# Performance work log

Measured on AMD Instinct MI355X. Metric: run time of the kernel, lower is better.

The kernel has to match this reference:

```python
import jax, jax.numpy as jnp
import numpy as np

EPS = 1e-8
LAM = 20.0  # lambda_softmax
I, R, T, W, D = 128, 48, 64, 100, 768


def l2norm(x, axis=-1):
    # matches torch l2norm: x / (sqrt(sum(x^2)) + eps)
    return x / (jnp.sqrt(jnp.sum(x * x, axis=axis, keepdims=True)) + EPS)


def _safe_div(num, den):
    return num / jnp.where(den > 0, den, 1.0)


def setup_inputs() -> dict:
    key = jax.random.key(0)
    k1, k2, k3, k4, k5 = jax.random.split(key, 5)
    return {
        "local_img_query": jax.random.normal(k1, (I, R, D), jnp.float32),
        "local_img_value": jax.random.normal(k2, (I, R, D), jnp.float32),
        "local_text_key": jax.random.normal(k3, (T, W, D), jnp.float32),
        "local_text_value": jax.random.normal(k4, (T, W, D), jnp.float32),
        "text_length": jax.random.randint(k5, (T,), 8, W + 1),
    }


def reference(local_img_query, local_img_value, local_text_key, local_text_value, text_length):
    # Vectorized over texts: padding words are masked instead of sliced,
    # reproducing the per-text ragged loop of compute_weiTexts exactly.
    Tn, Wn, Dn = local_text_key.shape
    In, Rn, _ = local_img_query.shape
    dtype = local_img_query.dtype
    mask = jnp.arange(Wn)[None, :] < text_length[:, None]          # [T,W] valid words
    Lf = text_length.astype(dtype)

    imgQn = l2norm(local_img_query)                                 # [I,R,D]
    txtKn = l2norm(local_text_key)                                  # [T,W,D]
    # cosine scores, shared by both directions (t2i uses the transpose)
    sim = jnp.einsum('twd,ird->tiwr', txtKn, imgQn)                 # [T,I,W,R]
    a = jax.nn.leaky_relu(sim, 0.1)

    # ---- i2t: query = image regions, source = text words ----
    ai = l2norm(a, axis=-1)                                         # l2norm over R per word row
    ai = jnp.swapaxes(ai, 2, 3)                                     # [T,I,R,W]
    m4 = mask[:, None, None, :]
    attn = jax.nn.softmax(jnp.where(m4, ai * LAM, -1e30), axis=-1)  # softmax over valid words
    attn = attn * m4
    # focal_equal with true source length L_i
    funcF = attn * Lf[:, None, None, None] - jnp.sum(attn, -1, keepdims=True)
    tmp = jnp.where(funcF > 0, attn, 0.0)
    attn = _safe_div(tmp, jnp.sum(tmp, -1, keepdims=True))
    weiText = l2norm(jnp.einsum('tirw,twd->tird', attn, local_text_value))  # [T,I,R,D]
    num = jnp.sum(local_img_value[None] * weiText, -1)
    den = jnp.maximum(jnp.linalg.norm(local_img_value, axis=-1)[None]
                      * jnp.linalg.norm(weiText, axis=-1), EPS)
    i2t = jnp.mean(num / den, axis=-1)                              # [T,I]

    # ---- t2i: query = text words, source = image regions ----
    a2 = jnp.swapaxes(a, 2, 3) * m4                                 # [T,I,R,W]; zero padded words before l2norm over W
    a2 = l2norm(a2, axis=-1)
    a2 = jnp.swapaxes(a2, 2, 3)                                     # [T,I,W,R]
    attn2 = jax.nn.softmax(a2 * LAM, axis=-1)                       # softmax over regions (dense)
    funcF2 = attn2 * Rn - jnp.sum(attn2, -1, keepdims=True)
    tmp2 = jnp.where(funcF2 > 0, attn2, 0.0)
    attn2 = _safe_div(tmp2, jnp.sum(tmp2, -1, keepdims=True))
    weiImage = l2norm(jnp.einsum('tiwr,ird->tiwd', attn2, local_img_value))  # [T,I,W,D]
    num2 = jnp.sum(local_text_value[:, None] * weiImage, -1)        # [T,I,W]
    den2 = jnp.maximum(jnp.linalg.norm(local_text_value, axis=-1)[:, None]
                       * jnp.linalg.norm(weiImage, axis=-1), EPS)
    sim2 = jnp.where(mask[:, None, :], num2 / den2, 0.0)
    t2i = jnp.sum(sim2, axis=-1) / Lf[:, None]                      # masked mean over valid words, [T,I]

    return i2t.T, t2i.T                                             # ([n_img,n_txt], [n_img,n_txt])
```

## Files before the change

### kernel.cpp

```cpp
#include <hip/hip_runtime.h>

#define EPS   1e-8f
#define LAMB  20.0f
#define NI    128
#define NR    48
#define NT    64
#define NW    100
#define ND    768

typedef unsigned int uint;
typedef unsigned short ushortt;
typedef __attribute__((ext_vector_type(8))) short short8;
typedef __attribute__((ext_vector_type(4))) float f32x4;

#define OFF_KHI  102400ULL
#define OFF_KLO  11112448ULL
#define OFF_QHI  22122496ULL
#define OFF_QLO  31559680ULL
#define OFF_TVB  40996864ULL
#define OFF_IVB  52006912ULL
#define OFF_MH   61444096ULL
#define OFF_ML   63279104ULL
#define OFF_HH   65114112ULL
#define OFF_HL   65900544ULL
#define WS_NEED  66686976ULL

__device__ inline unsigned short f2bf(float f) {
    uint u = __float_as_uint(f);
    u = (u + 0x7fffu + ((u >> 16) & 1u)) >> 16;
    return (unsigned short)u;
}
__device__ inline float bf2f(unsigned short h) {
    return __uint_as_float((uint)h << 16);
}
__device__ inline void split_store(float4 v, ushortt* hp, ushortt* lp) {
    unsigned short h0 = f2bf(v.x), h1 = f2bf(v.y), h2 = f2bf(v.z), h3 = f2bf(v.w);
    float f0 = bf2f(h0), f1 = bf2f(h1), f2 = bf2f(h2), f3 = bf2f(h3);
    ushort4 H; H.x = h0; H.y = h1; H.z = h2; H.w = h3;
    ushort4 L2; L2.x = f2bf(v.x - f0); L2.y = f2bf(v.y - f1); L2.z = f2bf(v.z - f2); L2.w = f2bf(v.w - f3);
    *(ushort4*)hp = H;
    *(ushort4*)lp = L2;
}
__device__ inline int swzATT(int r, int w) {
    return r * 128 + ((((w >> 3) ^ (r & 7)) << 3) | (w & 7));
}
__device__ inline int swzATT2(int w, int r) {
    return w * 64 + ((((r >> 3) ^ (w & 7)) << 3) | (r & 7));
}
__device__ inline float wredsum(float v) {
#pragma unroll
    for (int m = 1; m < 64; m <<= 1) v += __shfl_xor(v, m, 64);
    return v;
}
__device__ inline float wredmax(float v) {
#pragma unroll
    for (int m = 1; m < 64; m <<= 1) v = fmaxf(v, __shfl_xor(v, m, 64));
    return v;
}

__global__ void nafs_norms(const float* __restrict__ imgQ,
                           const float* __restrict__ imgV,
                           const float* __restrict__ txtK,
                           const float* __restrict__ txtV,
                           float* __restrict__ ws) {
    int row  = blockIdx.x * 4 + (threadIdx.x >> 6);
    int lane = threadIdx.x & 63;
    const float* src;
    int inv;
    if (row < 6144)       { src = imgQ + (size_t)row * ND;           inv = 1; }
    else if (row < 12544) { src = txtK + (size_t)(row - 6144) * ND;  inv = 1; }
    else if (row < 18688) { src = imgV + (size_t)(row - 12544) * ND; inv = 0; }
    else                  { src = txtV + (size_t)(row - 18688) * ND; inv = 0; }
    float ss = 0.f;
#pragma unroll
    for (int j = 0; j < 3; ++j) {
        float4 v = *(const float4*)(src + j * 256 + lane * 4);
        ss += v.x * v.x + v.y * v.y + v.z * v.z + v.w * v.w;
    }
#pragma unroll
    for (int off = 32; off > 0; off >>= 1) ss += __shfl_down(ss, off, 64);
    if (lane == 0) {
        float n = sqrtf(ss);
        ws[row] = inv ? (1.0f / (n + EPS)) : n;
    }
}

__global__ __launch_bounds__(256)
void nafs_convert(const float* __restrict__ txtK,
                  const float* __restrict__ imgQ,
                  const float* __restrict__ txtV,
                  const float* __restrict__ imgV,
                  const float* __restrict__ ws,
                  ushortt* __restrict__ khi, ushortt* __restrict__ klo,
                  ushortt* __restrict__ qhi, ushortt* __restrict__ qlo,
                  ushortt* __restrict__ tvb, ushortt* __restrict__ ivb) {
    __shared__ __align__(16) ushortt sH[24 * 512];
    __shared__ __align__(16) ushortt sL[24 * 512];
    const int blk = blockIdx.x;
    const int tid = threadIdx.x;

    const float* src;
    const float* scale = nullptr;
    ushortt* dh;
    ushortt* dl = nullptr;
    int rowbase, rowlimit;

    if (blk < 448) {
        int tile = blk, t = tile / 7, m = tile % 7;
        src = txtK + (size_t)t * NW * ND;
        scale = ws + 6144 + t * NW;
        dh = khi + (size_t)tile * 24 * 512;
        dl = klo + (size_t)tile * 24 * 512;
        rowbase = m * 16; rowlimit = NW;
    } else if (blk < 832) {
        int tile = blk - 448, i = tile / 3;
        src = imgQ + (size_t)i * NR * ND;
        scale = ws + i * NR;
        dh = qhi + (size_t)tile * 24 * 512;
        dl = qlo + (size_t)tile * 24 * 512;
        rowbase = (tile % 3) * 16; rowlimit = NR;
    } else if (blk < 1280) {
        int tile = blk - 832, t = tile / 7, m = tile % 7;
        src = txtV + (size_t)t * NW * ND;
        dh = tvb + (size_t)tile * 24 * 512;
        rowbase = m * 16; rowlimit = NW;
    } else {
        int tile = blk - 1280, i = tile / 3;
        src = imgV + (size_t)i * NR * ND;
        dh = ivb + (size_t)tile * 24 * 512;
        rowbase = (tile % 3) * 16; rowlimit = NR;
    }

#pragma unroll
    for (int j = 0; j < 12; ++j) {
        int idx = tid + j * 256;
        int l   = idx / 192;
        int c4  = idx % 192;
        int row = rowbase + l;
        int dc32 = c4 >> 3, quad = (c4 & 7) >> 1, j0 = (c4 & 1) * 4;
        int off  = dc32 * 512 + (quad * 16 + l) * 8 + j0;
        if (row < rowlimit) {
            float4 v = *(const float4*)(src + (size_t)row * ND + c4 * 4);
            if (scale) { float s = scale[row]; v.x *= s; v.y *= s; v.z *= s; v.w *= s; }
            if (dl) {
                split_store(v, &sH[off], &sL[off]);
            } else {
                ushort4 u; u.x = f2bf(v.x); u.y = f2bf(v.y); u.z = f2bf(v.z); u.w = f2bf(v.w);
                *(ushort4*)&sH[off] = u;
            }
        } else {
            ushort4 z; z.x = z.y = z.z = z.w = 0;
            *(ushort4*)&sH[off] = z;
            if (dl) *(ushort4*)&sL[off] = z;
        }
    }
    __syncthreads();
#pragma unroll
    for (int j = 0; j < 6; ++j) {
        int idx = tid + j * 256;
        *(short8*)&dh[idx * 8] = *(short8*)&sH[idx * 8];
        if (dl) *(short8*)&dl[idx * 8] = *(short8*)&sL[idx * 8];
    }
}

__global__ void nafs_gram_m(const ushortt* __restrict__ tvb,
                            ushortt* __restrict__ mh, ushortt* __restrict__ ml) {
    const int blk = blockIdx.x;
    const int t = blk / 7, m = blk % 7;
    const int tid = threadIdx.x, wv = tid >> 6, lane = tid & 63;
    const int quad = lane >> 4, l15 = lane & 15;
    const ushortt* base = tvb + (size_t)t * 7 * 24 * 512;
    ushortt* mhB = mh + (size_t)t * 7 * 4 * 512;
    ushortt* mlB = ml + (size_t)t * 7 * 4 * 512;

    const int n0 = wv, n1 = wv + 4;
    f32x4 c0 = (f32x4){0.f, 0.f, 0.f, 0.f};
    f32x4 c1 = (f32x4){0.f, 0.f, 0.f, 0.f};
    for (int dc32 = 0; dc32 < 24; ++dc32) {
        short8 av = *(const short8*)&base[((size_t)m * 24 + dc32) * 512 + lane * 8];
        short8 b0 = *(const short8*)&base[((size_t)n0 * 24 + dc32) * 512 + lane * 8];
        c0 = __builtin_amdgcn_mfma_f32_16x16x32_bf16(av, b0, c0, 0, 0, 0);
        if (n1 < 7) {
            short8 b1 = *(const short8*)&base[((size_t)n1 * 24 + dc32) * 512 + lane * 8];
            c1 = __builtin_amdgcn_mfma_f32_16x16x32_bf16(av, b1, c1, 0, 0, 0);
        }
    }
#pragma unroll
    for (int p = 0; p < 2; ++p) {
        int n = (p == 0) ? n0 : n1;
        if (n < 7) {
            f32x4 c = (p == 0) ? c0 : c1;
#pragma unroll
            for (int reg = 0; reg < 4; ++reg) {
                int wc = n * 16 + l15;
                int lrow = quad * 4 + reg;
                float v = c[reg];
                ushortt h = f2bf(v);
                size_t fo = ((size_t)m * 4 + (wc >> 5)) * 512
                          + ((((wc >> 3) & 3) * 16 + lrow) * 8) + (wc & 7);
                mhB[fo] = h;
                mlB[fo] = f2bf(v - bf2f(h));
            }
        }
    }
    for (int idx = tid; idx < 32; idx += 256) {
        int ln = 32 + idx;
        short8 z = (short8){0, 0, 0, 0, 0, 0, 0, 0};
        size_t fo = ((size_t)m * 4 + 3) * 512 + (size_t)ln * 8;
        *(short8*)&mhB[fo] = z; *(short8*)&mlB[fo] = z;
    }
}

__global__ void nafs_gram_h(const ushortt* __restrict__ ivb,
                            ushortt* __restrict__ hh, ushortt* __restrict__ hl) {
    const int i = blockIdx.x;
    const int tid = threadIdx.x, wv = tid >> 6, lane = tid & 63;
    const int quad = lane >> 4, l15 = lane & 15;
    const ushortt* base = ivb + (size_t)i * 3 * 24 * 512;
    ushortt* hhB = hh + (size_t)i * 3 * 2 * 512;
    ushortt* hlB = hl + (size_t)i * 3 * 2 * 512;
    if (wv < 3) {
        int m = wv;
        f32x4 c[3];
#pragma unroll
        for (int n = 0; n < 3; ++n) c[n] = (f32x4){0.f, 0.f, 0.f, 0.f};
        for (int dc32 = 0; dc32 < 24; ++dc32) {
            short8 av = *(const short8*)&base[((size_t)m * 24 + dc32) * 512 + lane * 8];
#pragma unroll
            for (int n = 0; n < 3; ++n) {
                short8 bv = *(const short8*)&base[((size_t)n * 24 + dc32) * 512 + lane * 8];
                c[n] = __builtin_amdgcn_mfma_f32_16x16x32_bf16(av, bv, c[n], 0, 0, 0);
            }
        }
#pragma unroll
        for (int n = 0; n < 3; ++n)
#pragma unroll
            for (int reg = 0; reg < 4; ++reg) {
                int rc = n * 16 + l15;
                int lrow = quad * 4 + reg;
                float v = c[n][reg];
                ushortt h = f2bf(v);
                size_t fo = ((size_t)m * 2 + (rc >> 5)) * 512
                          + ((((rc >> 3) & 3) * 16 + lrow) * 8) + (rc & 7);
                hhB[fo] = h;
                hlB[fo] = f2bf(v - bf2f(h));
            }
    }
    for (int idx = tid; idx < 3 * 32; idx += 256) {
        int m = idx >> 5, ln = 32 + (idx & 31);
        short8 z = (short8){0, 0, 0, 0, 0, 0, 0, 0};
        size_t fo = ((size_t)m * 2 + 1) * 512 + (size_t)ln * 8;
        *(short8*)&hhB[fo] = z; *(short8*)&hlB[fo] = z;
    }
}

__global__ __launch_bounds__(256, 2)
void nafs_fused3(const int*  __restrict__ tlen,
                 const float* __restrict__ ws,
                 const ushortt* __restrict__ khi, const ushortt* __restrict__ klo,
                 const ushortt* __restrict__ qhi, const ushortt* __restrict__ qlo,
                 const ushortt* __restrict__ tvb, const ushortt* __restrict__ ivb,
                 const ushortt* __restrict__ mh, const ushortt* __restrict__ ml,
                 const ushortt* __restrict__ hh, const ushortt* __restrict__ hl,
                 float* __restrict__ out) {
    __shared__ __align__(16) ushortt shATT[48 * 128];
    __shared__ __align__(16) ushortt shATT2[112 * 64];
    __shared__ __align__(16) ushortt shQ[2 * 9 * 512];
    __shared__ float sCol[NR], sSe1[NR], sS11[NR], sS21[NR];
    __shared__ float sCos1[NR], sCos2[112];
    __shared__ float sSS1[NR], sDD1[NR], sSS2[112], sDD2[112];

    const int tid  = threadIdx.x;
    const int wv   = tid >> 6;
    const int lane = tid & 63;
    const int quad = lane >> 4;
    const int l15  = lane & 15;
    const int key  = l15 & 7;
    const int b    = blockIdx.x;
    const int xcd  = b & 7;
    const int idx  = b >> 3;
    const int st   = idx >> 6;
    const int rem  = idx & 63;
    const int i    = (xcd << 4) | (rem >> 2);
    const int t    = (st << 2) | (rem & 3);
    const int L    = tlen[t];
    const float Lf = (float)L;

    const float* __restrict__ nVi = ws + 12544;
    const float* __restrict__ nVt = ws + 18688;

    if (tid < NR) {
        sSS1[tid] = 0.f; sDD1[tid] = 0.f;
        sCol[tid] = 0.f; sSe1[tid] = 0.f; sS11[tid] = 0.f; sS21[tid] = 0.f;
    }
    for (int idx2 = tid; idx2 < 112 * 2; idx2 += 256) {
        int w = idx2 >> 1, nb = 6 + (idx2 & 1);
        short8 z = (short8){0, 0, 0, 0, 0, 0, 0, 0};
        *(short8*)&shATT2[w * 64 + ((nb ^ (w & 7)) << 3)] = z;
    }

    const int m0  = wv, m1 = wv + 4;
    const int m1c = (m1 == 7) ? 6 : m1;
    const size_t kb0 = ((size_t)(t * 7 + m0)) * 24 * 512 + (size_t)lane * 8;
    const size_t kb1 = ((size_t)(t * 7 + m1c)) * 24 * 512 + (size_t)lane * 8;
    const size_t qb  = ((size_t)(i * 3)) * 24 * 512 + (size_t)lane * 8;
    const ushortt* fK0h = khi + kb0;
    const ushortt* fK0l = klo + kb0;
    const ushortt* fK1h = khi + kb1;
    const ushortt* fK1l = klo + kb1;
    const ushortt* fQh  = qhi + qb;
    const ushortt* fQl  = qlo + qb;
    const ushortt* fA0  = tvb + kb0;
    const ushortt* fA1  = tvb + kb1;
    const ushortt* fB   = ivb + qb;

    f32x4 acc[2][3];
    f32x4 gf[2][3];
#pragma unroll
    for (int a = 0; a < 2; ++a)
#pragma unroll
        for (int n = 0; n < 3; ++n) {
            acc[a][n] = (f32x4){0.f, 0.f, 0.f, 0.f};
            gf[a][n]  = (f32x4){0.f, 0.f, 0.f, 0.f};
        }

    short8 c0h = *(const short8*)(fK0h);
    short8 c0l = *(const short8*)(fK0l);
    short8 c1h = *(const short8*)(fK1h);
    short8 c1l = *(const short8*)(fK1l);
    short8 ct0 = *(const short8*)(fA0);
    short8 ct1 = *(const short8*)(fA1);
    {
        ushortt* dst = shQ + lane * 8;
        if (wv == 0) {
            *(short8*)(dst + 0 * 512) = *(const short8*)(fQh);
            *(short8*)(dst + 4 * 512) = *(const short8*)(fQh + 24576);
            *(short8*)(dst + 8 * 512) = *(const short8*)(fB + 24576);
        } else if (wv == 1) {
            *(short8*)(dst + 1 * 512) = *(const short8*)(fQl);
            *(short8*)(dst + 5 * 512) = *(const short8*)(fQl + 24576);
        } else if (wv == 2) {
            *(short8*)(dst + 2 * 512) = *(const short8*)(fQh + 12288);
            *(short8*)(dst + 6 * 512) = *(const short8*)(fB);
        } else {
            *(short8*)(dst + 3 * 512) = *(const short8*)(fQl + 12288);
            *(short8*)(dst + 7 * 512) = *(const short8*)(fB + 12288);
        }
    }
    __syncthreads();

    for (int dc32 = 0; dc32 < 24; ++dc32) {
        const int bb = dc32 & 1;
        short8 n0h, n0l, n1h, n1l, nt0, nt1;
        short8 s0, s1, s2;
        if (dc32 < 23) {
            const int o = (dc32 + 1) * 512;
            n0h = *(const short8*)(fK0h + o);
            n0l = *(const short8*)(fK0l + o);
            n1h = *(const short8*)(fK1h + o);
            n1l = *(const short8*)(fK1l + o);
            nt0 = *(const short8*)(fA0 + o);
            nt1 = *(const short8*)(fA1 + o);
            if (wv == 0) {
                s0 = *(const short8*)(fQh + o);
                s1 = *(const short8*)(fQh + 24576 + o);
                s2 = *(const short8*)(fB + 24576 + o);
            } else if (wv == 1) {
                s0 = *(const short8*)(fQl + o);
                s1 = *(const short8*)(fQl + 24576 + o);
            } else if (wv == 2) {
                s0 = *(const short8*)(fQh + 12288 + o);
                s1 = *(const short8*)(fB + o);
            } else {
                s0 = *(const short8*)(fQl + 12288 + o);
                s1 = *(const short8*)(fB + 12288 + o);
            }
        }
        {
            const ushortt* qs = shQ + bb * (9 * 512) + lane * 8;
#pragma unroll
            for (int n = 0; n < 3; ++n) {
                short8 bh = *(const short8*)(qs + (2 * n) * 512);
                short8 bl = *(const short8*)(qs + (2 * n + 1) * 512);
                short8 tB = *(const short8*)(qs + (6 + n) * 512);
                acc[0][n] = __builtin_amdgcn_mfma_f32_16x16x32_bf16(c0h, bh, acc[0][n], 0, 0, 0);
                acc[0][n] = __builtin_amdgcn_mfma_f32_16x16x32_bf16(c0h, bl, acc[0][n], 0, 0, 0);
                acc[0][n] = __builtin_amdgcn_mfma_f32_16x16x32_bf16(c0l, bh, acc[0][n], 0, 0, 0);
                acc[1][n] = __builtin_amdgcn_mfma_f32_16x16x32_bf16(c1h, bh, acc[1][n], 0, 0, 0);
                acc[1][n] = __builtin_amdgcn_mfma_f32_16x16x32_bf16(c1h, bl, acc[1][n], 0, 0, 0);
                acc[1][n] = __builtin_amdgcn_mfma_f32_16x16x32_bf16(c1l, bh, acc[1][n], 0, 0, 0);
                gf[0][n]  = __builtin_amdgcn_mfma_f32_16x16x32_bf16(ct0, tB, gf[0][n], 0, 0, 0);
                gf[1][n]  = __builtin_amdgcn_mfma_f32_16x16x32_bf16(ct1, tB, gf[1][n], 0, 0, 0);
            }
        }
        if (dc32 < 23) {
            ushortt* dst = shQ + (bb ^ 1) * (9 * 512) + lane * 8;
            if (wv == 0) {
                *(short8*)(dst + 0 * 512) = s0;
                *(short8*)(dst + 4 * 512) = s1;
                *(short8*)(dst + 8 * 512) = s2;
            } else if (wv == 1) {
                *(short8*)(dst + 1 * 512) = s0;
                *(short8*)(dst + 5 * 512) = s1;
            } else if (wv == 2) {
                *(short8*)(dst + 2 * 512) = s0;
                *(short8*)(dst + 6 * 512) = s1;
            } else {
                *(short8*)(dst + 3 * 512) = s0;
                *(short8*)(dst + 7 * 512) = s1;
            }
            c0h = n0h; c0l = n0l; c1h = n1h; c1l = n1l; ct0 = nt0; ct1 = nt1;
        }
        __syncthreads();
    }

    float lk[2][3][4];
#pragma unroll
    for (int a = 0; a < 2; ++a) {
        int m = wv + 4 * a;
        bool ok = (m < 7);
#pragma unroll
        for (int n = 0; n < 3; ++n)
#pragma unroll
            for (int reg = 0; reg < 4; ++reg) {
                float s = ok ? acc[a][n][reg] : 0.f;
                lk[a][n][reg] = (s > 0.f) ? s : 0.1f * s;
            }
    }

    float invW[2][4];
#pragma unroll
    for (int a = 0; a < 2; ++a)
#pragma unroll
        for (int reg = 0; reg < 4; ++reg) {
            float ss = 0.f;
#pragma unroll
            for (int n = 0; n < 3; ++n) ss = fmaf(lk[a][n][reg], lk[a][n][reg], ss);
            ss += __shfl_xor(ss, 1, 64); ss += __shfl_xor(ss, 2, 64);
            ss += __shfl_xor(ss, 4, 64); ss += __shfl_xor(ss, 8, 64);
            invW[a][reg] = 1.0f / (sqrtf(ss) + EPS);
        }

    float e1[2][3][4];
    {
        float cs[3] = {0.f, 0.f, 0.f}, es[3] = {0.f, 0.f, 0.f};
#pragma unroll
        for (int a = 0; a < 2; ++a) {
            int m = wv + 4 * a;
#pragma unroll
            for (int reg = 0; reg < 4; ++reg) {
                int w = m * 16 + quad * 4 + reg;
                bool act = (m < 7) && (w < L);
#pragma unroll
                for (int n = 0; n < 3; ++n) {
                    float v = lk[a][n][reg];
                    float e = act ? __expf(v * invW[a][reg] * LAMB) : 0.f;
                    e1[a][n][reg] = e;
                    if (act) cs[n] = fmaf(v, v, cs[n]);
                    es[n] += e;
                }
            }
        }
#pragma unroll
        for (int n = 0; n < 3; ++n) {
            float c = cs[n], e = es[n];
            c += __shfl_xor(c, 16, 64); c += __shfl_xor(c, 32, 64);
            e += __shfl_xor(e, 16, 64); e += __shfl_xor(e, 32, 64);
            if (quad == 0) {
                atomicAdd(&sCol[n * 16 + l15], c);
                atomicAdd(&sSe1[n * 16 + l15], e);
            }
        }
    }
    __syncthreads();

    {
        float inv2[3];
#pragma unroll
        for (int n = 0; n < 3; ++n) inv2[n] = 1.0f / (sqrtf(sCol[n * 16 + l15]) + EPS);
#pragma unroll
        for (int a = 0; a < 2; ++a) {
            int m = wv + 4 * a;
            if (m < 7) {
#pragma unroll
                for (int reg = 0; reg < 4; ++reg) {
                    int w = m * 16 + quad * 4 + reg;
                    float e2[3];
                    float se = 0.f;
#pragma unroll
                    for (int n = 0; n < 3; ++n) {
                        float e = __expf(lk[a][n][reg] * inv2[n] * LAMB);
                        e2[n] = e; se += e;
                    }
                    se += __shfl_xor(se, 1, 64); se += __shfl_xor(se, 2, 64);
                    se += __shfl_xor(se, 4, 64); se += __shfl_xor(se, 8, 64);
                    float inv = 1.0f / se;
                    float S1 = e2[0] * inv + e2[1] * inv + e2[2] * inv;
                    S1 += __shfl_xor(S1, 1, 64); S1 += __shfl_xor(S1, 2, 64);
                    S1 += __shfl_xor(S1, 4, 64); S1 += __shfl_xor(S1, 8, 64);
                    float sel[3];
                    float S2 = 0.f;
#pragma unroll
                    for (int n = 0; n < 3; ++n) {
                        float p = e2[n] * inv;
                        sel[n] = ((p * 48.0f - S1) > 0.f) ? p : 0.f;
                        S2 += sel[n];
                    }
                    S2 += __shfl_xor(S2, 1, 64); S2 += __shfl_xor(S2, 2, 64);
                    S2 += __shfl_xor(S2, 4, 64); S2 += __shfl_xor(S2, 8, 64);
                    float iS2 = 1.0f / ((S2 > 0.f) ? S2 : 1.0f);
                    bool rowOK = (w < L);
#pragma unroll
                    for (int n = 0; n < 3; ++n) {
                        float val = rowOK ? sel[n] * iS2 : 0.f;
                        shATT2[swzATT2(w, n * 16 + l15)] = f2bf(val);
                    }
                }
            }
        }
    }

    float invSe[3];
#pragma unroll
    for (int n = 0; n < 3; ++n) invSe[n] = 1.0f / sSe1[n * 16 + l15];
    {
        float s1p[3] = {0.f, 0.f, 0.f};
#pragma unroll
        for (int a = 0; a < 2; ++a)
#pragma unroll
            for (int n = 0; n < 3; ++n)
#pragma unroll
                for (int reg = 0; reg < 4; ++reg)
                    s1p[n] += e1[a][n][reg] * invSe[n];
#pragma unroll
        for (int n = 0; n < 3; ++n) {
            float v = s1p[n];
            v += __shfl_xor(v, 16, 64); v += __shfl_xor(v, 32, 64);
            if (quad == 0) atomicAdd(&sS11[n * 16 + l15], v);
        }
    }
    __syncthreads();

    {
        float s2p[3] = {0.f, 0.f, 0.f};
#pragma unroll
        for (int n = 0; n < 3; ++n) {
            float S1r = sS11[n * 16 + l15];
#pragma unroll
            for (int a = 0; a < 2; ++a)
#pragma unroll
                for (int reg = 0; reg < 4; ++reg) {
                    float p = e1[a][n][reg] * invSe[n];
                    s2p[n] += ((p * Lf - S1r) > 0.f) ? p : 0.f;
                }
        }
#pragma unroll
        for (int n = 0; n < 3; ++n) {
            float v = s2p[n];
            v += __shfl_xor(v, 16, 64); v += __shfl_xor(v, 32, 64);
            if (quad == 0) atomicAdd(&sS21[n * 16 + l15], v);
        }
    }
    __syncthreads();

    {
#pragma unroll
        for (int n = 0; n < 3; ++n) {
            int r = n * 16 + l15;
            float S1r = sS11[r];
            float s2  = sS21[r];
            float iS2 = 1.0f / ((s2 > 0.f) ? s2 : 1.0f);
#pragma unroll
            for (int a = 0; a < 2; ++a) {
                int m = wv + 4 * a;
                ushortt v4[4];
#pragma unroll
                for (int reg = 0; reg < 4; ++reg) {
                    float p  = e1[a][n][reg] * invSe[n];
                    float tm = ((p * Lf - S1r) > 0.f) ? p : 0.f;
                    v4[reg] = f2bf(tm * iS2);
                }
                int wb = m * 16 + quad * 4;
                int f  = (((wb >> 3) ^ (r & 7)) << 3) | (wb & 7);
                *(ushort4*)&shATT[r * 128 + f] = *(ushort4*)v4;
            }
        }
    }
    __syncthreads();

    {
        float pd1[3] = {0.f, 0.f, 0.f};
#pragma unroll
        for (int a = 0; a < 2; ++a) {
            int m = wv + 4 * a;
            if (m < 7) {
#pragma unroll
                for (int reg = 0; reg < 4; ++reg) {
                    int w = m * 16 + quad * 4 + reg;
                    float p2 = 0.f;
#pragma unroll
                    for (int n = 0; n < 3; ++n) {
                        int r = n * 16 + l15;
                        float gv = gf[a][n][reg];
                        p2 = fmaf(gv, bf2f(shATT2[swzATT2(w, r)]), p2);
                        pd1[n] = fmaf(gv, bf2f(shATT[swzATT(r, w)]), pd1[n]);
                    }
                    p2 += __shfl_xor(p2, 1, 64); p2 += __shfl_xor(p2, 2, 64);
                    p2 += __shfl_xor(p2, 4, 64); p2 += __shfl_xor(p2, 8, 64);
                    if (l15 == 0) sDD2[w] = p2;
                }
            }
        }
#pragma unroll
        for (int n = 0; n < 3; ++n) {
            float p = pd1[n];
            p += __shfl_xor(p, 16, 64); p += __shfl_xor(p, 32, 64);
            if (quad == 0) atomicAdd(&sDD1[n * 16 + l15], p);
        }
    }

    {
        short8 af[3][4];
#pragma unroll
        for (int mt = 0; mt < 3; ++mt)
#pragma unroll
            for (int ks = 0; ks < 4; ++ks)
                af[mt][ks] = *(const short8*)&shATT[(mt * 16 + l15) * 128 + (((ks * 4 + quad) ^ key) << 3)];
        float ps[3][4];
#pragma unroll
        for (int mt = 0; mt < 3; ++mt)
#pragma unroll
            for (int reg = 0; reg < 4; ++reg) ps[mt][reg] = 0.f;
#pragma unroll
        for (int p = 0; p < 2; ++p) {
            int nt = wv + 4 * p;
            if (nt < 7) {
                const ushortt* pMh = mh + ((size_t)(t * 7 + nt)) * 4 * 512 + (size_t)lane * 8;
                const ushortt* pMl = ml + ((size_t)(t * 7 + nt)) * 4 * 512 + (size_t)lane * 8;
                short8 bh[4], bl[4];
#pragma unroll
                for (int ks = 0; ks < 4; ++ks) {
                    bh[ks] = *(const short8*)(pMh + ks * 512);
                    bl[ks] = *(const short8*)(pMl + ks * 512);
                }
                f32x4 y[3];
#pragma unroll
                for (int mt = 0; mt < 3; ++mt) y[mt] = (f32x4){0.f, 0.f, 0.f, 0.f};
#pragma unroll
                for (int mt = 0; mt < 3; ++mt)
#pragma unroll
                    for (int ks = 0; ks < 4; ++ks) {
                        y[mt] = __builtin_amdgcn_mfma_f32_16x16x32_bf16(af[mt][ks], bh[ks], y[mt], 0, 0, 0);
                        y[mt] = __builtin_amdgcn_mfma_f32_16x16x32_bf16(af[mt][ks], bl[ks], y[mt], 0, 0, 0);
                    }
                int wc = nt * 16 + l15;
#pragma unroll
                for (int mt = 0; mt < 3; ++mt)
#pragma unroll
                    for (int reg = 0; reg < 4; ++reg) {
                        int r = mt * 16 + quad * 4 + reg;
                        ps[mt][reg] = fmaf(y[mt][reg], bf2f(shATT[swzATT(r, wc)]), ps[mt][reg]);
                    }
            }
        }
#pragma unroll
        for (int mt = 0; mt < 3; ++mt)
#pragma unroll
            for (int reg = 0; reg < 4; ++reg) {
                float p = ps[mt][reg];
                p += __shfl_xor(p, 1, 64); p += __shfl_xor(p, 2, 64);
                p += __shfl_xor(p, 4, 64); p += __shfl_xor(p, 8, 64);
                if (l15 == 0) atomicAdd(&sSS1[mt * 16 + quad * 4 + reg], p);
            }
    }

    {
        short8 zbh[3][2], zbl[3][2];
#pragma unroll
        for (int n = 0; n < 3; ++n) {
#pragma unroll
            for (int ks = 0; ks < 2; ++ks) {
                size_t fo = (((size_t)(i * 3 + n)) * 2 + ks) * 512 + (size_t)lane * 8;
                zbh[n][ks] = *(const short8*)&hh[fo];
                zbl[n][ks] = *(const short8*)&hl[fo];
            }
        }
#pragma unroll
        for (int a = 0; a < 2; ++a) {
            int m = wv + 4 * a;
            if (m < 7) {
                f32x4 z[3];
#pragma unroll
                for (int n = 0; n < 3; ++n) z[n] = (f32x4){0.f, 0.f, 0.f, 0.f};
#pragma unroll
                for (int ks = 0; ks < 2; ++ks) {
                    short8 a2f = *(const short8*)&shATT2[(m * 16 + l15) * 64 + (((ks * 4 + quad) ^ key) << 3)];
#pragma unroll
                    for (int n = 0; n < 3; ++n) {
                        z[n] = __builtin_amdgcn_mfma_f32_16x16x32_bf16(a2f, zbh[n][ks], z[n], 0, 0, 0);
                        z[n] = __builtin_amdgcn_mfma_f32_16x16x32_bf16(a2f, zbl[n][ks], z[n], 0, 0, 0);
                    }
                }
#pragma unroll
                for (int reg = 0; reg < 4; ++reg) {
                    int w = m * 16 + quad * 4 + reg;
                    float p = 0.f;
#pragma unroll
                    for (int n = 0; n < 3; ++n)
                        p = fmaf(z[n][reg], bf2f(shATT2[swzATT2(w, n * 16 + l15)]), p);
                    p += __shfl_xor(p, 1, 64); p += __shfl_xor(p, 2, 64);
                    p += __shfl_xor(p, 4, 64); p += __shfl_xor(p, 8, 64);
                    if (l15 == 0) sSS2[w] = p;
                }
            }
        }
    }
    __syncthreads();

    if (tid < NR) {
        float s = fmaxf(sSS1[tid], 0.f), d = sDD1[tid];
        float nu  = sqrtf(s);
        float num = d / (nu + EPS);
        float den = fmaxf(nVi[i * NR + tid] * (nu / (nu + EPS)), EPS);
        sCos1[tid] = num / den;
    } else if (tid >= 64 && tid < 176) {
        int w = tid - 64;
        if (w < L) {
            float s = fmaxf(sSS2[w], 0.f), d = sDD2[w];
            float nu  = sqrtf(s);
            float num = d / (nu + EPS);
            float den = fmaxf(nVt[t * NW + w] * (nu / (nu + EPS)), EPS);
            sCos2[w] = num / den;
        }
    }
    __syncthreads();
    if (tid == 0) {
        float s = 0.f;
        for (int r = 0; r < NR; ++r) s += sCos1[r];
        out[i * NT + t] = s * (1.0f / 48.0f);
    } else if (tid == 64) {
        float s = 0.f;
        for (int w = 0; w < L; ++w) s += sCos2[w];
        out[NI * NT + i * NT + t] = s / Lf;
    }
}

#define A_KH   0
#define A_KL   4480
#define A_QH   8960
#define A_QL   10880
#define A_ATT  0
#define A_ATT2 6528
#define SHA_SZ 14592
#define B1_TVT 3200
#define B2_IVT 6656
#define SHB_SZ 4900

__global__ __launch_bounds__(256, 3)
void nafs_fused_fb(const float* __restrict__ imgQ,
                   const float* __restrict__ imgV,
                   const float* __restrict__ txtK,
                   const float* __restrict__ txtV,
                   const int*  __restrict__ tlen,
                   const float* __restrict__ ws,
                   float* __restrict__ out) {
    __shared__ ushortt shA[SHA_SZ];
    __shared__ float shB[SHB_SZ];
    __shared__ float sKs[NW], sQs[NR], sInvW[NW], sInv2[NR], sCos1[NR], sCos2[112];

    const int tid  = threadIdx.x;
    const int wv   = tid >> 6;
    const int lane = tid & 63;
    const int quad = lane >> 4;
    const int l15  = lane & 15;
    const int b    = blockIdx.x;
    const int t    = b >> 7;
    const int i    = b & 127;
    const int L    = tlen[t];
    const float Lf = (float)L;

    const float* __restrict__ invQ = ws;
    const float* __restrict__ invK = ws + 6144;
    const float* __restrict__ nVi  = ws + 12544;
    const float* __restrict__ nVt  = ws + 18688;

    const float* Kbase  = txtK + (size_t)t * (NW * ND);
    const float* Qbase  = imgQ + (size_t)i * (NR * ND);
    const float* TVbase = txtV + (size_t)t * (NW * ND);
    const float* IVbase = imgV + (size_t)i * (NR * ND);

    if (tid < NW)                  sKs[tid]       = invK[t * NW + tid];
    else if (tid < NW + NR)        sQs[tid - NW]  = invQ[i * NR + (tid - NW)];

    const int mt0 = wv * 2, mt1 = wv * 2 + 1;
    f32x4 acc[2][3];
#pragma unroll
    for (int a = 0; a < 2; ++a)
#pragma unroll
        for (int n = 0; n < 3; ++n) acc[a][n] = (f32x4){0.f, 0.f, 0.f, 0.f};

    for (int dc = 0; dc < ND; dc += 32) {
        __syncthreads();
        for (int idx = tid; idx < 112 * 8; idx += 256) {
            int w = idx >> 3, seg = idx & 7;
            float4 v;
            if (w < NW) {
                v = *(const float4*)(Kbase + (size_t)w * ND + dc + seg * 4);
                float s = sKs[w];
                v.x *= s; v.y *= s; v.z *= s; v.w *= s;
            } else { v.x = v.y = v.z = v.w = 0.f; }
            split_store(v, &shA[A_KH + w * 40 + seg * 4], &shA[A_KL + w * 40 + seg * 4]);
        }
        for (int idx = tid; idx < NR * 8; idx += 256) {
            int r = idx >> 3, seg = idx & 7;
            float4 v = *(const float4*)(Qbase + (size_t)r * ND + dc + seg * 4);
            float s = sQs[r];
            v.x *= s; v.y *= s; v.z *= s; v.w *= s;
            split_store(v, &shA[A_QH + r * 40 + seg * 4], &shA[A_QL + r * 40 + seg * 4]);
        }
        __syncthreads();
        short8 bh[3], bl[3];
#pragma unroll
        for (int n = 0; n < 3; ++n) {
            bh[n] = *(const short8*)&shA[A_QH + (n * 16 + l15) * 40 + quad * 8];
            bl[n] = *(const short8*)&shA[A_QL + (n * 16 + l15) * 40 + quad * 8];
        }
#pragma unroll
        for (int a = 0; a < 2; ++a) {
            int m = (a == 0) ? mt0 : mt1;
            if (m < 7) {
                short8 ah = *(const short8*)&shA[A_KH + (m * 16 + l15) * 40 + quad * 8];
                short8 al = *(const short8*)&shA[A_KL + (m * 16 + l15) * 40 + quad * 8];
#pragma unroll
                for (int n = 0; n < 3; ++n) {
                    acc[a][n] = __builtin_amdgcn_mfma_f32_16x16x32_bf16(ah, bh[n], acc[a][n], 0, 0, 0);
                    acc[a][n] = __builtin_amdgcn_mfma_f32_16x16x32_bf16(ah, bl[n], acc[a][n], 0, 0, 0);
                    acc[a][n] = __builtin_amdgcn_mfma_f32_16x16x32_bf16(al, bh[n], acc[a][n], 0, 0, 0);
                }
            }
        }
    }
    __syncthreads();
#pragma unroll
    for (int a = 0; a < 2; ++a) {
        int m = (a == 0) ? mt0 : mt1;
        if (m < 7) {
#pragma unroll
            for (int n = 0; n < 3; ++n)
#pragma unroll
                for (int reg = 0; reg < 4; ++reg) {
                    int w = m * 16 + quad * 4 + reg;
                    if (w < NW) {
                        float s = acc[a][n][reg];
                        shB[w * 49 + n * 16 + l15] = (s > 0.f) ? s : 0.1f * s;
                    }
                }
        }
    }
    __syncthreads();

    if (tid < NW) {
        float ssum = 0.f;
#pragma unroll 8
        for (int r = 0; r < NR; ++r) { float v = shB[tid * 49 + r]; ssum += v * v; }
        sInvW[tid] = 1.0f / (sqrtf(ssum) + EPS);
    } else if (tid >= 128 && tid < 128 + NR) {
        int r = tid - 128;
        float ssum = 0.f;
        for (int w = 0; w < L; ++w) { float v = shB[w * 49 + r]; ssum += v * v; }
        sInv2[r] = 1.0f / (sqrtf(ssum) + EPS);
    }
    __syncthreads();

    for (int r = wv; r < NR; r += 4) {
        int w1 = lane, w2 = lane + 64;
        int v1ok = (w1 < L), v2ok = (w2 < L);
        float v1 = v1ok ? shB[w1 * 49 + r] * sInvW[w1] * LAMB : -1e30f;
        float v2 = v2ok ? shB[w2 * 49 + r] * sInvW[w2] * LAMB : -1e30f;
        float m  = wredmax(fmaxf(v1, v2));
        float e1 = v1ok ? expf(v1 - m) : 0.f;
        float e2 = v2ok ? expf(v2 - m) : 0.f;
        float inv = 1.0f / wredsum(e1 + e2);
        float p1 = e1 * inv, p2 = e2 * inv;
        float S1 = wredsum(p1 + p2);
        float t1 = ((p1 * Lf - S1) > 0.f) ? p1 : 0.f;
        float t2 = ((p2 * Lf - S1) > 0.f) ? p2 : 0.f;
        float S2 = wredsum(t1 + t2);
        float iS2 = 1.0f / ((S2 > 0.f) ? S2 : 1.0f);
        shA[A_ATT + r * 136 + w1] = f2bf(t1 * iS2);
        shA[A_ATT + r * 136 + w2] = f2bf(t2 * iS2);
    }
    for (int w = wv; w < L; w += 4) {
        int rok = (lane < NR);
        float v = rok ? shB[w * 49 + lane] * sInv2[lane] * LAMB : -1e30f;
        float m = wredmax(v);
        float e = rok ? expf(v - m) : 0.f;
        float inv = 1.0f / wredsum(e);
        float p = e * inv;
        float S1 = wredsum(p);
        float tm = ((p * 48.0f - S1) > 0.f) ? p : 0.f;
        float S2 = wredsum(tm);
        float iS2 = 1.0f / ((S2 > 0.f) ? S2 : 1.0f);
        shA[A_ATT2 + w * 72 + lane] = f2bf(tm * iS2);
    }
    for (int w = L + wv; w < 112; w += 4) shA[A_ATT2 + w * 72 + lane] = 0;
    __syncthreads();

    ushortt* shBu = (ushortt*)shB;
    const int kk = (L + 31) >> 5;
    float ss1[4] = {0.f, 0.f, 0.f, 0.f}, dd1[4] = {0.f, 0.f, 0.f, 0.f};
    const int mt = wv;
    const int cgrp = tid >> 5, ccol = tid & 31;

    for (int cc = 0; cc < ND; cc += 32) {
        __syncthreads();
        for (int w = cgrp; w < 128; w += 8) {
            float val = (w < NW) ? TVbase[(size_t)w * ND + cc + ccol] : 0.f;
            shBu[B1_TVT + ccol * 136 + w] = f2bf(val);
        }
        for (int idx = tid; idx < NR * 8; idx += 256) {
            int r = idx >> 3, seg = idx & 7;
            float4 v = *(const float4*)(IVbase + (size_t)r * ND + cc + seg * 4);
            float* p = &shB[r * 33 + seg * 4];
            p[0] = v.x; p[1] = v.y; p[2] = v.z; p[3] = v.w;
        }
        __syncthreads();
        if (mt < 3) {
            f32x4 u[2] = {(f32x4){0.f,0.f,0.f,0.f}, (f32x4){0.f,0.f,0.f,0.f}};
            for (int ks = 0; ks < kk; ++ks) {
                short8 a = *(const short8*)&shA[A_ATT + (mt * 16 + l15) * 136 + ks * 32 + quad * 8];
#pragma unroll
                for (int n = 0; n < 2; ++n) {
                    short8 bb = *(const short8*)&shBu[B1_TVT + (n * 16 + l15) * 136 + ks * 32 + quad * 8];
                    u[n] = __builtin_amdgcn_mfma_f32_16x16x32_bf16(a, bb, u[n], 0, 0, 0);
                }
            }
#pragma unroll
            for (int n = 0; n < 2; ++n)
#pragma unroll
                for (int reg = 0; reg < 4; ++reg) {
                    int r = mt * 16 + quad * 4 + reg;
                    float uu = u[n][reg];
                    ss1[reg] = fmaf(uu, uu, ss1[reg]);
                    dd1[reg] = fmaf(uu, shB[r * 33 + n * 16 + l15], dd1[reg]);
                }
        }
    }
    if (mt < 3) {
#pragma unroll
        for (int reg = 0; reg < 4; ++reg) {
            float s = ss1[reg], d = dd1[reg];
#pragma unroll
            for (int m = 1; m < 16; m <<= 1) { s += __shfl_xor(s, m, 64); d += __shfl_xor(d, m, 64); }
            if (l15 == 0) {
                int r = mt * 16 + quad * 4 + reg;
                float nu  = sqrtf(s);
                float num = d / (nu + EPS);
                float den = fmaxf(nVi[i * NR + r] * (nu / (nu + EPS)), EPS);
                sCos1[r] = num / den;
            }
        }
    }

    const int ntot = (L + 15) >> 4;
    float ss2[2] = {0.f, 0.f}, dd2[2] = {0.f, 0.f};

    for (int cc = 0; cc < ND; cc += 32) {
        __syncthreads();
        for (int idx = tid; idx < NW * 8; idx += 256) {
            int w = idx >> 3, seg = idx & 7;
            float4 v = *(const float4*)(TVbase + (size_t)w * ND + cc + seg * 4);
            float* p = &shB[w * 33 + seg * 4];
            p[0] = v.x; p[1] = v.y; p[2] = v.z; p[3] = v.w;
        }
        for (int r = cgrp; r < 64; r += 8) {
            float val = (r < NR) ? IVbase[(size_t)r * ND + cc + ccol] : 0.f;
            shBu[B2_IVT + ccol * 72 + r] = f2bf(val);
        }
        __syncthreads();
#pragma unroll
        for (int pp = 0; pp < 2; ++pp) {
            int nt = wv + 4 * pp;
            if (nt < ntot) {
                f32x4 u[2] = {(f32x4){0.f,0.f,0.f,0.f}, (f32x4){0.f,0.f,0.f,0.f}};
#pragma unroll
                for (int ks = 0; ks < 2; ++ks) {
                    short8 bb = *(const short8*)&shA[A_ATT2 + (nt * 16 + l15) * 72 + ks * 32 + quad * 8];
#pragma unroll
                    for (int mm = 0; mm < 2; ++mm) {
                        short8 aa = *(const short8*)&shBu[B2_IVT + (mm * 16 + l15) * 72 + ks * 32 + quad * 8];
                        u[mm] = __builtin_amdgcn_mfma_f32_16x16x32_bf16(aa, bb, u[mm], 0, 0, 0);
                    }
                }
                int w = nt * 16 + l15;
                float tvok = (w < L) ? 1.f : 0.f;
#pragma unroll
                for (int mm = 0; mm < 2; ++mm)
#pragma unroll
                    for (int reg = 0; reg < 4; ++reg) {
                        int c = mm * 16 + quad * 4 + reg;
                        float uu = u[mm][reg];
                        float tv = (w < L) ? shB[w * 33 + c] : 0.f;
                        ss2[pp] = fmaf(uu, uu, ss2[pp]);
                        dd2[pp] = fmaf(uu, tv * tvok, dd2[pp]);
                    }
            }
        }
    }
#pragma unroll
    for (int pp = 0; pp < 2; ++pp) {
        int nt = wv + 4 * pp;
        if (nt < ntot) {
            float s = ss2[pp], d = dd2[pp];
            s += __shfl_xor(s, 16, 64); d += __shfl_xor(d, 16, 64);
            s += __shfl_xor(s, 32, 64); d += __shfl_xor(d, 32, 64);
            if (quad == 0) {
                int w = nt * 16 + l15;
                if (w < L) {
                    float nu  = sqrtf(s);
                    float num = d / (nu + EPS);
                    float den = fmaxf(nVt[t * NW + w] * (nu / (nu + EPS)), EPS);
                    sCos2[w] = num / den;
                }
            }
        }
    }
    __syncthreads();
    if (tid == 0) {
        float s = 0.f;
        for (int r = 0; r < NR; ++r) s += sCos1[r];
        out[i * NT + t] = s * (1.0f / 48.0f);
    } else if (tid == 64) {
        float s = 0.f;
        for (int w = 0; w < L; ++w) s += sCos2[w];
        out[NI * NT + i * NT + t] = s / Lf;
    }
}

extern "C" void kernel_launch(void* const* d_in, const int* in_sizes, int n_in,
                              void* d_out, int out_size, void* d_ws, size_t ws_size,
                              hipStream_t stream) {
    (void)in_sizes; (void)n_in; (void)out_size;
    const float* imgQ = (const float*)d_in[0];
    const float* imgV = (const float*)d_in[1];
    const float* txtK = (const float*)d_in[2];
    const float* txtV = (const float*)d_in[3];
    const int*   tlen = (const int*)d_in[4];
    float* ws  = (float*)d_ws;
    float* out = (float*)d_out;

    hipLaunchKernelGGL(nafs_norms, dim3(6272), dim3(256), 0, stream,
                       imgQ, imgV, txtK, txtV, ws);

    if (ws_size >= WS_NEED) {
        char* base = (char*)d_ws;
        ushortt* khi = (ushortt*)(base + OFF_KHI);
        ushortt* klo = (ushortt*)(base + OFF_KLO);
        ushortt* qhi = (ushortt*)(base + OFF_QHI);
        ushortt* qlo = (ushortt*)(base + OFF_QLO);
        ushortt* tvb = (ushortt*)(base + OFF_TVB);
        ushortt* ivb = (ushortt*)(base + OFF_IVB);
        ushortt* mh  = (ushortt*)(base + OFF_MH);
        ushortt* ml  = (ushortt*)(base + OFF_ML);
        ushortt* hh  = (ushortt*)(base + OFF_HH);
        ushortt* hl  = (ushortt*)(base + OFF_HL);
        hipLaunchKernelGGL(nafs_convert, dim3(1664), dim3(256), 0, stream,
                           txtK, imgQ, txtV, imgV, ws, khi, klo, qhi, qlo, tvb, ivb);
        hipLaunchKernelGGL(nafs_gram_m, dim3(448), dim3(256), 0, stream, tvb, mh, ml);
        hipLaunchKernelGGL(nafs_gram_h, dim3(128), dim3(256), 0, stream, ivb, hh, hl);
        hipLaunchKernelGGL(nafs_fused3, dim3(NT * NI), dim3(256), 0, stream,
                           tlen, ws, khi, klo, qhi, qlo, tvb, ivb, mh, ml, hh, hl, out);
    } else {
        hipLaunchKernelGGL(nafs_fused_fb, dim3(NT * NI), dim3(256), 0, stream,
                           imgQ, imgV, txtK, txtV, tlen, ws, out);
    }
}
```

Measured before the change: 627.6 us.

## Deepen K/A prefetch to two stages, hoist M loads, use softmax sum identity

The main GEMM loop now prefetches K and text-value fragments two iterations ahead instead of one, to hide more global-load latency. The M-matrix fragment loads are moved ahead of the pd1 computation so their latency overlaps with earlier work. The row sum of the softmax is replaced by the constant 1 in the focal thresholds, which drops one shared atomic reduction and one barrier. This raises register pressure under launch_bounds(256,2), and thresholds computed against 1.0 can differ slightly from the computed sum because of rounding.

```diff
diff --git a/kernel.cpp b/kernel.cpp
--- a/kernel.cpp
+++ b/kernel.cpp
@@ -266,7 +266,7 @@
     __shared__ __align__(16) ushortt shATT[48 * 128];
     __shared__ __align__(16) ushortt shATT2[112 * 64];
     __shared__ __align__(16) ushortt shQ[2 * 9 * 512];
-    __shared__ float sCol[NR], sSe1[NR], sS11[NR], sS21[NR];
+    __shared__ float sCol[NR], sSe1[NR], sS21[NR];
     __shared__ float sCos1[NR], sCos2[112];
     __shared__ float sSS1[NR], sDD1[NR], sSS2[112], sDD2[112];
 
@@ -291,7 +291,7 @@
 
     if (tid < NR) {
         sSS1[tid] = 0.f; sDD1[tid] = 0.f;
-        sCol[tid] = 0.f; sSe1[tid] = 0.f; sS11[tid] = 0.f; sS21[tid] = 0.f;
+        sCol[tid] = 0.f; sSe1[tid] = 0.f; sS21[tid] = 0.f;
     }
     for (int idx2 = tid; idx2 < 112 * 2; idx2 += 256) {
         int w = idx2 >> 1, nb = 6 + (idx2 & 1);
@@ -330,6 +330,12 @@
     short8 c1l = *(const short8*)(fK1l);
     short8 ct0 = *(const short8*)(fA0);
     short8 ct1 = *(const short8*)(fA1);
+    short8 d0h = *(const short8*)(fK0h + 512);
+    short8 d0l = *(const short8*)(fK0l + 512);
+    short8 d1h = *(const short8*)(fK1h + 512);
+    short8 d1l = *(const short8*)(fK1l + 512);
+    short8 dt0 = *(const short8*)(fA0 + 512);
+    short8 dt1 = *(const short8*)(fA1 + 512);
     {
         ushortt* dst = shQ + lane * 8;
         if (wv == 0) {
@@ -351,16 +357,19 @@
 
     for (int dc32 = 0; dc32 < 24; ++dc32) {
         const int bb = dc32 & 1;
-        short8 n0h, n0l, n1h, n1l, nt0, nt1;
+        short8 x0h, x0l, x1h, x1l, xt0, xt1;
         short8 s0, s1, s2;
+        if (dc32 < 22) {
+            const int o = (dc32 + 2) * 512;
+            x0h = *(const short8*)(fK0h + o);
+            x0l = *(const short8*)(fK0l + o);
+            x1h = *(const short8*)(fK1h + o);
+            x1l = *(const short8*)(fK1l + o);
+            xt0 = *(const short8*)(fA0 + o);
+            xt1 = *(const short8*)(fA1 + o);
+        }
         if (dc32 < 23) {
             const int o = (dc32 + 1) * 512;
-            n0h = *(const short8*)(fK0h + o);
-            n0l = *(const short8*)(fK0l + o);
-            n1h = *(const short8*)(fK1h + o);
-            n1l = *(const short8*)(fK1l + o);
-            nt0 = *(const short8*)(fA0 + o);
-            nt1 = *(const short8*)(fA1 + o);
             if (wv == 0) {
                 s0 = *(const short8*)(fQh + o);
                 s1 = *(const short8*)(fQh + 24576 + o);
@@ -409,7 +418,10 @@
                 *(short8*)(dst + 3 * 512) = s0;
                 *(short8*)(dst + 7 * 512) = s1;
             }
-            c0h = n0h; c0l = n0l; c1h = n1h; c1l = n1l; ct0 = nt0; ct1 = nt1;
+        }
+        c0h = d0h; c0l = d0l; c1h = d1h; c1l = d1l; ct0 = dt0; ct1 = dt1;
+        if (dc32 < 22) {
+            d0h = x0h; d0l = x0l; d1h = x1h; d1l = x1l; dt0 = xt0; dt1 = xt1;
         }
         __syncthreads();
     }
@@ -495,15 +507,12 @@
                     se += __shfl_xor(se, 1, 64); se += __shfl_xor(se, 2, 64);
                     se += __shfl_xor(se, 4, 64); se += __shfl_xor(se, 8, 64);
                     float inv = 1.0f / se;
-                    float S1 = e2[0] * inv + e2[1] * inv + e2[2] * inv;
-                    S1 += __shfl_xor(S1, 1, 64); S1 += __shfl_xor(S1, 2, 64);
-                    S1 += __shfl_xor(S1, 4, 64); S1 += __shfl_xor(S1, 8, 64);
                     float sel[3];
                     float S2 = 0.f;
 #pragma unroll
                     for (int n = 0; n < 3; ++n) {
                         float p = e2[n] * inv;
-                        sel[n] = ((p * 48.0f - S1) > 0.f) ? p : 0.f;
+                        sel[n] = ((p * 48.0f - 1.0f) > 0.f) ? p : 0.f;
                         S2 += sel[n];
                     }
                     S2 += __shfl_xor(S2, 1, 64); S2 += __shfl_xor(S2, 2, 64);
@@ -524,34 +533,15 @@
 #pragma unroll
     for (int n = 0; n < 3; ++n) invSe[n] = 1.0f / sSe1[n * 16 + l15];
     {
-        float s1p[3] = {0.f, 0.f, 0.f};
-#pragma unroll
-        for (int a = 0; a < 2; ++a)
-#pragma unroll
-            for (int n = 0; n < 3; ++n)
-#pragma unroll
-                for (int reg = 0; reg < 4; ++reg)
-                    s1p[n] += e1[a][n][reg] * invSe[n];
+        float s2p[3] = {0.f, 0.f, 0.f};
 #pragma unroll
         for (int n = 0; n < 3; ++n) {
-            float v = s1p[n];
-            v += __shfl_xor(v, 16, 64); v += __shfl_xor(v, 32, 64);
-            if (quad == 0) atomicAdd(&sS11[n * 16 + l15], v);
-        }
-    }
-    __syncthreads();
-
-    {
-        float s2p[3] = {0.f, 0.f, 0.f};
-#pragma unroll
-        for (int n = 0; n < 3; ++n) {
-            float S1r = sS11[n * 16 + l15];
 #pragma unroll
             for (int a = 0; a < 2; ++a)
 #pragma unroll
                 for (int reg = 0; reg < 4; ++reg) {
                     float p = e1[a][n][reg] * invSe[n];
-                    s2p[n] += ((p * Lf - S1r) > 0.f) ? p : 0.f;
+                    s2p[n] += ((p * Lf - 1.0f) > 0.f) ? p : 0.f;
                 }
         }
 #pragma unroll
@@ -567,7 +557,6 @@
 #pragma unroll
         for (int n = 0; n < 3; ++n) {
             int r = n * 16 + l15;
-            float S1r = sS11[r];
             float s2  = sS21[r];
             float iS2 = 1.0f / ((s2 > 0.f) ? s2 : 1.0f);
 #pragma unroll
@@ -577,7 +566,7 @@
 #pragma unroll
                 for (int reg = 0; reg < 4; ++reg) {
                     float p  = e1[a][n][reg] * invSe[n];
-                    float tm = ((p * Lf - S1r) > 0.f) ? p : 0.f;
+                    float tm = ((p * Lf - 1.0f) > 0.f) ? p : 0.f;
                     v4[reg] = f2bf(tm * iS2);
                 }
                 int wb = m * 16 + quad * 4;
@@ -587,6 +576,20 @@
         }
     }
     __syncthreads();
+
+    short8 ybh[2][4], ybl[2][4];
+#pragma unroll
+    for (int p = 0; p < 2; ++p) {
+        int nt = wv + 4 * p;
+        int ntc = (nt == 7) ? 6 : nt;
+        const ushortt* pMh = mh + ((size_t)(t * 7 + ntc)) * 4 * 512 + (size_t)lane * 8;
+        const ushortt* pMl = ml + ((size_t)(t * 7 + ntc)) * 4 * 512 + (size_t)lane * 8;
+#pragma unroll
+        for (int ks = 0; ks < 4; ++ks) {
+            ybh[p][ks] = *(const short8*)(pMh + ks * 512);
+            ybl[p][ks] = *(const short8*)(pMl + ks * 512);
+        }
+    }
 
     {
         float pd1[3] = {0.f, 0.f, 0.f};
@@ -635,14 +638,6 @@
         for (int p = 0; p < 2; ++p) {
             int nt = wv + 4 * p;
             if (nt < 7) {
-                const ushortt* pMh = mh + ((size_t)(t * 7 + nt)) * 4 * 512 + (size_t)lane * 8;
-                const ushortt* pMl = ml + ((size_t)(t * 7 + nt)) * 4 * 512 + (size_t)lane * 8;
-                short8 bh[4], bl[4];
-#pragma unroll
-                for (int ks = 0; ks < 4; ++ks) {
-                    bh[ks] = *(const short8*)(pMh + ks * 512);
-                    bl[ks] = *(const short8*)(pMl + ks * 512);
-                }
                 f32x4 y[3];
 #pragma unroll
                 for (int mt = 0; mt < 3; ++mt) y[mt] = (f32x4){0.f, 0.f, 0.f, 0.f};
@@ -650,8 +645,8 @@
                 for (int mt = 0; mt < 3; ++mt)
 #pragma unroll
                     for (int ks = 0; ks < 4; ++ks) {
-                        y[mt] = __builtin_amdgcn_mfma_f32_16x16x32_bf16(af[mt][ks], bh[ks], y[mt], 0, 0, 0);
-                        y[mt] = __builtin_amdgcn_mfma_f32_16x16x32_bf16(af[mt][ks], bl[ks], y[mt], 0, 0, 0);
+                        y[mt] = __builtin_amdgcn_mfma_f32_16x16x32_bf16(af[mt][ks], ybh[p][ks], y[mt], 0, 0, 0);
+                        y[mt] = __builtin_amdgcn_mfma_f32_16x16x32_bf16(af[mt][ks], ybl[p][ks], y[mt], 0, 0, 0);
                     }
                 int wc = nt * 16 + l15;
 #pragma unroll
```

Result: slower. 755.1 us (+20.3%).
